# Performance work log

Hardware: AMD Instinct MI355X
Metric: run time of the kernel (lower is better)

The kernel has to match this reference:

```python
import jax, jax.numpy as jnp
import numpy as np

COMMITMENT_COST = 0.25


def _mlp(x, Ws, bs):
    # Linear layers with ReLU between hidden layers, linear output (rlpyt-style MlpModel).
    n = len(Ws)
    for i in range(n):
        x = x @ Ws[i] + bs[i]
        if i < n - 1:
            x = jax.nn.relu(x)
    return x


def setup_inputs() -> dict:
    key = jax.random.key(0)
    ks = jax.random.split(key, 16)
    B, D_in, H1, H2, D_code, K = 16384, 1024, 2048, 1024, 256, 1024

    def lin(kw, kb, fan_in, fan_out):
        lim = 1.0 / np.sqrt(fan_in)
        W = jax.random.uniform(kw, (fan_in, fan_out), jnp.float32, -lim, lim)
        b = jax.random.uniform(kb, (fan_out,), jnp.float32, -lim, lim)
        return W, b

    enc_W1, enc_b1 = lin(ks[0], ks[1], D_in, H1)
    enc_W2, enc_b2 = lin(ks[2], ks[3], H1, H2)
    enc_W3, enc_b3 = lin(ks[4], ks[5], H2, D_code)
    dec_W1, dec_b1 = lin(ks[6], ks[7], D_code, H2)
    dec_W2, dec_b2 = lin(ks[8], ks[9], H2, H1)
    dec_W3, dec_b3 = lin(ks[10], ks[11], H1, D_in)
    codebook = jax.random.uniform(ks[12], (K, D_code), jnp.float32, -1.0 / K, 1.0 / K)
    x = jax.random.normal(ks[13], (B, D_in), jnp.float32)
    return {
        "x": x,
        "enc_W1": enc_W1, "enc_b1": enc_b1,
        "enc_W2": enc_W2, "enc_b2": enc_b2,
        "enc_W3": enc_W3, "enc_b3": enc_b3,
        "codebook": codebook,
        "dec_W1": dec_W1, "dec_b1": dec_b1,
        "dec_W2": dec_W2, "dec_b2": dec_b2,
        "dec_W3": dec_W3, "dec_b3": dec_b3,
    }


def reference(x, enc_W1, enc_b1, enc_W2, enc_b2, enc_W3, enc_b3, codebook,
              dec_W1, dec_b1, dec_W2, dec_b2, dec_W3, dec_b3):
    # Encoder MLP -> z: [B, D_code]
    z = _mlp(x, [enc_W1, enc_W2, enc_W3], [enc_b1, enc_b2, enc_b3])
    # Squared L2 distances z vs codebook: [B, K]
    distances = (jnp.sum(z * z, axis=1, keepdims=True)
                 + jnp.sum(codebook * codebook, axis=1)
                 - 2.0 * jnp.einsum('bd,kd->bk', z, codebook))
    indices = jnp.argmin(distances, axis=1)  # [B]
    # one-hot scatter + matmul in the original == direct gather
    quantized = codebook[indices]            # [B, D_code]
    # training-mode losses
    e_latent_loss = jnp.mean((jax.lax.stop_gradient(quantized) - z) ** 2)
    q_latent_loss = jnp.mean((quantized - jax.lax.stop_gradient(z)) ** 2)
    loss = q_latent_loss + COMMITMENT_COST * e_latent_loss
    # straight-through estimator
    quantized_st = z + jax.lax.stop_gradient(quantized - z)
    reconstructed = _mlp(quantized_st, [dec_W1, dec_W2, dec_W3], [dec_b1, dec_b2, dec_b3])
    return reconstructed, quantized_st, loss, indices[:, None]
```

## Files before the change

### kernel.cpp

```cpp
#include <hip/hip_runtime.h>
#include <hip/hip_bf16.h>
#include <stdint.h>


#define BDIM  16384
#define DIN   1024
#define DH1   2048
#define DH2   1024
#define DCODE 256
#define KCODE 1024

typedef __hip_bfloat16 bf16;
typedef __attribute__((ext_vector_type(8))) short short8;
typedef __attribute__((ext_vector_type(4))) float f32x4;

__device__ __forceinline__ void gload16(const void* g, void* l)
{
    __builtin_amdgcn_global_load_lds(
        (const __attribute__((address_space(1))) unsigned int*)g,
        (__attribute__((address_space(3))) unsigned int*)l, 16, 0, 0);
}

__device__ __forceinline__ void split3(float f, ushort* h, ushort* m, ushort* l)
{
    bf16 bh = __float2bfloat16(f);
    float r1 = f - __bfloat162float(bh);
    bf16 bm = __float2bfloat16(r1);
    float r2 = r1 - __bfloat162float(bm);
    bf16 bl = __float2bfloat16(r2);
    *h = *(ushort*)&bh; *m = *(ushort*)&bm; *l = *(ushort*)&bl;
}

template<int RELU, int OUTK>
__global__ __launch_bounds__(512, 2)
void gemms(const ushort* __restrict__ Apl, const ushort* __restrict__ Bpl,
           const float* __restrict__ bias, void* __restrict__ C,
           void* __restrict__ C2,
           int M, int N, int K, size_t PA, size_t PB, size_t PC)
{
    __shared__ __align__(16) short As[2][3][128][32];
    __shared__ __align__(16) short Bs[2][3][128][32];
    const int tid  = threadIdx.x;
    const int lane = tid & 63;
    const int wave = tid >> 6;
    const int wm = (wave >> 1) << 5;
    const int wn = (wave & 1) << 6;
    const int fr = lane & 15, fq = lane >> 4;
    const int row0 = blockIdx.y << 7, col0 = blockIdx.x << 7;

    const int srow = (wave << 4) + (lane >> 2);
    const int sslot = lane & 3;
    const int skg = (sslot ^ ((srow >> 1) & 3)) << 3;

    const ushort* AgT = Apl + (size_t)(row0 + srow) * K + skg;
    const ushort* BgT = Bpl + (size_t)(col0 + srow) * K + skg;

    f32x4  acc[2][4];
    double dacc[2][4][4];
    #pragma unroll
    for (int i = 0; i < 2; ++i)
        #pragma unroll
        for (int j = 0; j < 4; ++j) {
            acc[i][j] = (f32x4)0.0f;
            #pragma unroll
            for (int r = 0; r < 4; ++r) dacc[i][j][r] = 0.0;
        }

    auto stage = [&](int b, int kb) {
        #pragma unroll
        for (int p = 0; p < 3; ++p) {
            gload16(AgT + (size_t)p * PA + kb, &As[b][p][wave << 4][0]);
            gload16(BgT + (size_t)p * PB + kb, &Bs[b][p][wave << 4][0]);
        }
    };

    stage(0, 0);
    const int nsteps = K >> 5;
    for (int s = 0; s < nsteps; ++s) {
        const int b = s & 1;
        if (s + 1 < nsteps) {
            stage(b ^ 1, (s + 1) << 5);
            asm volatile("s_waitcnt vmcnt(6)" ::: "memory");
        } else {
            asm volatile("s_waitcnt vmcnt(0)" ::: "memory");
        }
        __builtin_amdgcn_s_barrier();
        __builtin_amdgcn_sched_barrier(0);

        short8 bh[4], bm[4], bl[4];
        #pragma unroll
        for (int j = 0; j < 4; ++j) {
            const int bn = wn + (j << 4) + fr;
            const int bsl = (fq ^ ((bn >> 1) & 3)) << 3;
            bh[j] = *(const short8*)&Bs[b][0][bn][bsl];
            bm[j] = *(const short8*)&Bs[b][1][bn][bsl];
            bl[j] = *(const short8*)&Bs[b][2][bn][bsl];
        }
        #pragma unroll
        for (int i = 0; i < 2; ++i) {
            const int an = wm + (i << 4) + fr;
            const int asl = (fq ^ ((an >> 1) & 3)) << 3;
            short8 ah = *(const short8*)&As[b][0][an][asl];
            short8 am = *(const short8*)&As[b][1][an][asl];
            short8 al = *(const short8*)&As[b][2][an][asl];
            #pragma unroll
            for (int j = 0; j < 4; ++j) {
                acc[i][j] = __builtin_amdgcn_mfma_f32_16x16x32_bf16(ah, bh[j], acc[i][j], 0, 0, 0);
                acc[i][j] = __builtin_amdgcn_mfma_f32_16x16x32_bf16(ah, bm[j], acc[i][j], 0, 0, 0);
                acc[i][j] = __builtin_amdgcn_mfma_f32_16x16x32_bf16(am, bh[j], acc[i][j], 0, 0, 0);
                acc[i][j] = __builtin_amdgcn_mfma_f32_16x16x32_bf16(ah, bl[j], acc[i][j], 0, 0, 0);
                acc[i][j] = __builtin_amdgcn_mfma_f32_16x16x32_bf16(al, bh[j], acc[i][j], 0, 0, 0);
                acc[i][j] = __builtin_amdgcn_mfma_f32_16x16x32_bf16(am, bm[j], acc[i][j], 0, 0, 0);
            }
        }

        if (s & 1) {
            #pragma unroll
            for (int i = 0; i < 2; ++i)
                #pragma unroll
                for (int j = 0; j < 4; ++j) {
                    #pragma unroll
                    for (int r = 0; r < 4; ++r) dacc[i][j][r] += (double)acc[i][j][r];
                    acc[i][j] = (f32x4)0.0f;
                }
        }
        __builtin_amdgcn_sched_barrier(0);
        __builtin_amdgcn_s_barrier();
    }
    #pragma unroll
    for (int i = 0; i < 2; ++i)
        #pragma unroll
        for (int j = 0; j < 4; ++j)
            #pragma unroll
            for (int r = 0; r < 4; ++r) dacc[i][j][r] += (double)acc[i][j][r];

    #pragma unroll
    for (int j = 0; j < 4; ++j) {
        const int n = col0 + wn + (j << 4) + fr;
        const double bv = (double)bias[n];
        #pragma unroll
        for (int i = 0; i < 2; ++i) {
            const int mb = row0 + wm + (i << 4) + (fq << 2);
            #pragma unroll
            for (int r = 0; r < 4; ++r) {
                double v = dacc[i][j][r] + bv;
                if (RELU) v = v > 0.0 ? v : 0.0;
                const size_t o = (size_t)(mb + r) * N + n;
                if (OUTK == 2 || OUTK == 3) ((double*)C)[o] = v;
                if (OUTK == 0 || OUTK == 3) {
                    ushort h, m, l;
                    split3((float)v, &h, &m, &l);
                    ushort* Cp = (ushort*)((OUTK == 0) ? C : C2);
                    Cp[o] = h; Cp[PC + o] = m; Cp[2 * PC + o] = l;
                }
            }
        }
    }
}

__global__ __launch_bounds__(512, 2)
void distm(const ushort* __restrict__ Zpl, const ushort* __restrict__ Cpl,
           const double* __restrict__ c2, double* __restrict__ psc,
           int* __restrict__ pix)
{
    __shared__ __align__(16) short As[3][128][40];
    __shared__ __align__(16) short Bs[3][128][40];
    const int tid  = threadIdx.x;
    const int lane = tid & 63;
    const int wave = tid >> 6;
    const int wm = (wave >> 1) << 5;
    const int wn = (wave & 1) << 6;
    const int fr = lane & 15, fq = lane >> 4;
    const int row0 = blockIdx.y << 7, col0 = blockIdx.x << 7;
    const int sr = tid >> 2, sc = (tid & 3) << 3;
    const size_t PZ = (size_t)BDIM * DCODE;
    const size_t PC = (size_t)KCODE * DCODE;

    const ushort* Ag = Zpl + (size_t)(row0 + sr) * DCODE + sc;
    const ushort* Bg = Cpl + (size_t)(col0 + sr) * DCODE + sc;

    f32x4  acc[2][4];
    double dacc[2][4][4];
    #pragma unroll
    for (int i = 0; i < 2; ++i)
        #pragma unroll
        for (int j = 0; j < 4; ++j) {
            acc[i][j] = (f32x4)0.0f;
            #pragma unroll
            for (int r = 0; r < 4; ++r) dacc[i][j][r] = 0.0;
        }

    short8 sa[3], sb[3];
    #pragma unroll
    for (int p = 0; p < 3; ++p) {
        sa[p] = *(const short8*)(Ag + (size_t)p * PZ);
        sb[p] = *(const short8*)(Bg + (size_t)p * PC);
    }

    const int nsteps = DCODE >> 5;
    for (int s = 0; s < nsteps; ++s) {
        __syncthreads();
        #pragma unroll
        for (int p = 0; p < 3; ++p) {
            *(short8*)&As[p][sr][sc] = sa[p];
            *(short8*)&Bs[p][sr][sc] = sb[p];
        }
        __syncthreads();
        if (s + 1 < nsteps) {
            const int kb = (s + 1) << 5;
            #pragma unroll
            for (int p = 0; p < 3; ++p) {
                sa[p] = *(const short8*)(Ag + (size_t)p * PZ + kb);
                sb[p] = *(const short8*)(Bg + (size_t)p * PC + kb);
            }
        }

        short8 bh[4], bm[4], bl[4];
        #pragma unroll
        for (int j = 0; j < 4; ++j) {
            const int bn = wn + (j << 4) + fr;
            bh[j] = *(const short8*)&Bs[0][bn][fq << 3];
            bm[j] = *(const short8*)&Bs[1][bn][fq << 3];
            bl[j] = *(const short8*)&Bs[2][bn][fq << 3];
        }
        #pragma unroll
        for (int i = 0; i < 2; ++i) {
            const int an = wm + (i << 4) + fr;
            short8 ah = *(const short8*)&As[0][an][fq << 3];
            short8 am = *(const short8*)&As[1][an][fq << 3];
            short8 al = *(const short8*)&As[2][an][fq << 3];
            #pragma unroll
            for (int j = 0; j < 4; ++j) {
                acc[i][j] = __builtin_amdgcn_mfma_f32_16x16x32_bf16(ah, bh[j], acc[i][j], 0, 0, 0);
                acc[i][j] = __builtin_amdgcn_mfma_f32_16x16x32_bf16(ah, bm[j], acc[i][j], 0, 0, 0);
                acc[i][j] = __builtin_amdgcn_mfma_f32_16x16x32_bf16(am, bh[j], acc[i][j], 0, 0, 0);
                acc[i][j] = __builtin_amdgcn_mfma_f32_16x16x32_bf16(ah, bl[j], acc[i][j], 0, 0, 0);
                acc[i][j] = __builtin_amdgcn_mfma_f32_16x16x32_bf16(al, bh[j], acc[i][j], 0, 0, 0);
                acc[i][j] = __builtin_amdgcn_mfma_f32_16x16x32_bf16(am, bm[j], acc[i][j], 0, 0, 0);
            }
        }

        if (s & 1) {
            #pragma unroll
            for (int i = 0; i < 2; ++i)
                #pragma unroll
                for (int j = 0; j < 4; ++j) {
                    #pragma unroll
                    for (int r = 0; r < 4; ++r) dacc[i][j][r] += (double)acc[i][j][r];
                    acc[i][j] = (f32x4)0.0f;
                }
        }
    }
    #pragma unroll
    for (int i = 0; i < 2; ++i)
        #pragma unroll
        for (int j = 0; j < 4; ++j)
            #pragma unroll
            for (int r = 0; r < 4; ++r) dacc[i][j][r] += (double)acc[i][j][r];

    __syncthreads();
    double* scb = (double*)&As[0][0][0];
    int*    sib = (int*)(scb + 256);

    #pragma unroll
    for (int i = 0; i < 2; ++i) {
        #pragma unroll
        for (int r = 0; r < 4; ++r) {
            double bs = 1e300; int bi = 0;
            #pragma unroll
            for (int j = 0; j < 4; ++j) {
                const int n = col0 + wn + (j << 4) + fr;
                const double s = c2[n] - 2.0 * dacc[i][j][r];
                if (s < bs) { bs = s; bi = n; }
            }
            #pragma unroll
            for (int msk = 1; msk < 16; msk <<= 1) {
                double os = __shfl_xor(bs, msk, 64);
                int    oi = __shfl_xor(bi, msk, 64);
                if (os < bs || (os == bs && oi < bi)) { bs = os; bi = oi; }
            }
            if (fr == 0) {
                const int lr = wm + (i << 4) + (fq << 2) + r;
                scb[lr * 2 + (wave & 1)] = bs;
                sib[lr * 2 + (wave & 1)] = bi;
            }
        }
    }
    __syncthreads();
    if (tid < 128) {
        double s0 = scb[tid * 2], s1 = scb[tid * 2 + 1];
        int    i0 = sib[tid * 2], i1 = sib[tid * 2 + 1];
        const bool t1 = (s1 < s0) || (s1 == s0 && i1 < i0);
        const size_t o = (size_t)(row0 + tid) * (KCODE / 128) + blockIdx.x;
        psc[o] = t1 ? s1 : s0;
        pix[o] = t1 ? i1 : i0;
    }
}

__global__ __launch_bounds__(256)
void reduce8(const double* __restrict__ psc, const int* __restrict__ pix,
             int* __restrict__ idx_out)
{
    const int row = blockIdx.x * 256 + threadIdx.x;
    const double* ps = psc + (size_t)row * (KCODE / 128);
    const int*    pi = pix + (size_t)row * (KCODE / 128);
    double m = ps[0]; int mi = pi[0];
    #pragma unroll
    for (int t = 1; t < KCODE / 128; ++t) {
        double s = ps[t]; int c = pi[t];
        if (s < m || (s == m && c < mi)) { m = s; mi = c; }
    }
    idx_out[row] = mi;
}

template<int RELU, int OUTBF>
__global__ __launch_bounds__(256)
void gemmb2(const ushort* __restrict__ A, const ushort* __restrict__ Bt,
            const float* __restrict__ bias, void* __restrict__ C,
            int M, int N, int K)
{
    __shared__ __align__(16) short As[2][128][32];
    __shared__ __align__(16) short Bs[2][128][32];
    const int tid  = threadIdx.x;
    const int lane = tid & 63;
    const int wave = tid >> 6;
    const int wm = (wave >> 1) << 6, wn = (wave & 1) << 6;
    const int fr = lane & 15;
    const int fq = lane >> 4;
    const int row0 = blockIdx.y << 7, col0 = blockIdx.x << 7;

    const int sr0 = (wave << 5) + (lane >> 2);
    const int sslot = lane & 3;
    const int kg0 = (sslot ^ ((sr0 >> 1) & 3)) << 3;
    const int sr1 = sr0 + 16;
    const int kg1 = (sslot ^ ((sr1 >> 1) & 3)) << 3;

    const ushort* Ag0 = A  + (size_t)(row0 + sr0) * K + kg0;
    const ushort* Ag1 = A  + (size_t)(row0 + sr1) * K + kg1;
    const ushort* Bg0 = Bt + (size_t)(col0 + sr0) * K + kg0;
    const ushort* Bg1 = Bt + (size_t)(col0 + sr1) * K + kg1;

    f32x4 acc[4][4];
    #pragma unroll
    for (int i = 0; i < 4; ++i)
        #pragma unroll
        for (int j = 0; j < 4; ++j) acc[i][j] = (f32x4)0.0f;

    auto stage = [&](int b, int kb) {
        gload16(Ag0 + kb, &As[b][wave << 5][0]);
        gload16(Ag1 + kb, &As[b][(wave << 5) + 16][0]);
        gload16(Bg0 + kb, &Bs[b][wave << 5][0]);
        gload16(Bg1 + kb, &Bs[b][(wave << 5) + 16][0]);
    };

    stage(0, 0);
    const int nsteps = K >> 5;
    for (int s = 0; s < nsteps; ++s) {
        const int b = s & 1;
        if (s + 1 < nsteps) {
            stage(b ^ 1, (s + 1) << 5);
            asm volatile("s_waitcnt vmcnt(4)" ::: "memory");
        } else {
            asm volatile("s_waitcnt vmcnt(0)" ::: "memory");
        }
        __builtin_amdgcn_s_barrier();
        __builtin_amdgcn_sched_barrier(0);

        short8 af[4], bf[4];
        #pragma unroll
        for (int i = 0; i < 4; ++i) {
            const int an = wm + (i << 4) + fr;
            af[i] = *(const short8*)&As[b][an][(fq ^ ((an >> 1) & 3)) << 3];
        }
        #pragma unroll
        for (int j = 0; j < 4; ++j) {
            const int bn = wn + (j << 4) + fr;
            bf[j] = *(const short8*)&Bs[b][bn][(fq ^ ((bn >> 1) & 3)) << 3];
        }
        #pragma unroll
        for (int i = 0; i < 4; ++i)
            #pragma unroll
            for (int j = 0; j < 4; ++j)
                acc[i][j] = __builtin_amdgcn_mfma_f32_16x16x32_bf16(
                                af[i], bf[j], acc[i][j], 0, 0, 0);

        __builtin_amdgcn_sched_barrier(0);
        __builtin_amdgcn_s_barrier();
    }

    #pragma unroll
    for (int j = 0; j < 4; ++j) {
        const int n = col0 + wn + (j << 4) + fr;
        const float bv = bias[n];
        #pragma unroll
        for (int i = 0; i < 4; ++i) {
            const int mb = row0 + wm + (i << 4) + (fq << 2);
            #pragma unroll
            for (int r = 0; r < 4; ++r) {
                float v = acc[i][j][r] + bv;
                if (RELU) v = fmaxf(v, 0.0f);
                size_t o = (size_t)(mb + r) * N + n;
                if (OUTBF) ((bf16*)C)[o]  = __float2bfloat16(v);
                else       ((float*)C)[o] = v;
            }
        }
    }
}

__global__ __launch_bounds__(256)
void wtrans(const float* __restrict__ W, ushort* __restrict__ Wt, int K, int N)
{
    __shared__ float tile[64][65];
    const int tid = threadIdx.x;
    const int kb = blockIdx.y << 6, nb = blockIdx.x << 6;
    const int r = tid >> 4, c4 = (tid & 15) << 2;
    #pragma unroll
    for (int s = 0; s < 4; ++s) {
        float4 v = *(const float4*)(W + (size_t)(kb + r + (s << 4)) * N + nb + c4);
        tile[r + (s << 4)][c4 + 0] = v.x; tile[r + (s << 4)][c4 + 1] = v.y;
        tile[r + (s << 4)][c4 + 2] = v.z; tile[r + (s << 4)][c4 + 3] = v.w;
    }
    __syncthreads();
    #pragma unroll
    for (int s = 0; s < 4; ++s) {
        const int n = r + (s << 4);
        ushort u[4];
        #pragma unroll
        for (int l = 0; l < 4; ++l) {
            bf16 h = __float2bfloat16(tile[c4 + l][n]);
            u[l] = *(ushort*)&h;
        }
        *(ushort4*)(Wt + (size_t)(nb + n) * K + kb + c4) = make_ushort4(u[0], u[1], u[2], u[3]);
    }
}

__global__ __launch_bounds__(256)
void wsplit(const float* __restrict__ W, ushort* __restrict__ Wt, int K, int N)
{
    __shared__ float tile[64][65];
    const int tid = threadIdx.x;
    const int kb = blockIdx.y << 6, nb = blockIdx.x << 6;
    const int r = tid >> 4, c4 = (tid & 15) << 2;
    const size_t NK = (size_t)N * K;
    #pragma unroll
    for (int s = 0; s < 4; ++s) {
        float4 v = *(const float4*)(W + (size_t)(kb + r + (s << 4)) * N + nb + c4);
        tile[r + (s << 4)][c4 + 0] = v.x; tile[r + (s << 4)][c4 + 1] = v.y;
        tile[r + (s << 4)][c4 + 2] = v.z; tile[r + (s << 4)][c4 + 3] = v.w;
    }
    __syncthreads();
    #pragma unroll
    for (int s = 0; s < 4; ++s) {
        const int n = r + (s << 4);
        ushort h[4], m[4], l[4];
        #pragma unroll
        for (int e = 0; e < 4; ++e) split3(tile[c4 + e][n], &h[e], &m[e], &l[e]);
        const size_t o = (size_t)(nb + n) * K + kb + c4;
        *(ushort4*)(Wt + o)          = make_ushort4(h[0], h[1], h[2], h[3]);
        *(ushort4*)(Wt + NK + o)     = make_ushort4(m[0], m[1], m[2], m[3]);
        *(ushort4*)(Wt + 2 * NK + o) = make_ushort4(l[0], l[1], l[2], l[3]);
    }
}

__global__ __launch_bounds__(256)
void xsplit(const float* __restrict__ X, ushort* __restrict__ Xp, size_t P)
{
    const size_t i = ((size_t)blockIdx.x * 256 + threadIdx.x) << 2;
    float4 v = *(const float4*)(X + i);
    ushort h[4], m[4], l[4];
    split3(v.x, &h[0], &m[0], &l[0]);
    split3(v.y, &h[1], &m[1], &l[1]);
    split3(v.z, &h[2], &m[2], &l[2]);
    split3(v.w, &h[3], &m[3], &l[3]);
    *(ushort4*)(Xp + i)         = make_ushort4(h[0], h[1], h[2], h[3]);
    *(ushort4*)(Xp + P + i)     = make_ushort4(m[0], m[1], m[2], m[3]);
    *(ushort4*)(Xp + 2 * P + i) = make_ushort4(l[0], l[1], l[2], l[3]);
}

__global__ __launch_bounds__(64)
void c2_k(const float* __restrict__ cb, double* __restrict__ c2)
{
    int code = blockIdx.x, l = threadIdx.x;
    float4 v = *(const float4*)(cb + (size_t)code * DCODE + (l << 2));
    double s = (double)v.x * v.x + (double)v.y * v.y
             + (double)v.z * v.z + (double)v.w * v.w;
    #pragma unroll
    for (int off = 32; off; off >>= 1) s += __shfl_down(s, off, 64);
    if (l == 0) c2[code] = s;
}

__global__ __launch_bounds__(256)
void gather_k(const int* __restrict__ idx_in, const float* __restrict__ cb,
              const double* __restrict__ z, ushort* __restrict__ qstb,
              float* __restrict__ out_qst, float* __restrict__ out_idx,
              double* __restrict__ psum)
{
    const int tid  = threadIdx.x;
    const int row  = (blockIdx.x << 2) + (tid >> 6);
    const int lane = tid & 63;
    const int d    = lane << 2;
    const int idx  = idx_in[row];

    float4 qv = *(const float4*)(cb + (size_t)idx * DCODE + d);
    const double* zp = z + (size_t)row * DCODE + d;
    double2 z0 = *(const double2*)(zp);
    double2 z1 = *(const double2*)(zp + 2);

    double q[4] = {(double)qv.x, (double)qv.y, (double)qv.z, (double)qv.w};
    double zz[4] = {z0.x, z0.y, z1.x, z1.y};
    double qs[4];
    double s = 0.0;
    #pragma unroll
    for (int e = 0; e < 4; ++e) {
        double diff = q[e] - zz[e];
        qs[e] = zz[e] + diff;
        s += diff * diff;
    }
    *(float4*)(out_qst + (size_t)row * DCODE + d) =
        make_float4((float)qs[0], (float)qs[1], (float)qs[2], (float)qs[3]);
    ushort u[4];
    #pragma unroll
    for (int e = 0; e < 4; ++e) {
        bf16 h = __float2bfloat16((float)qs[e]);
        u[e] = *(ushort*)&h;
    }
    *(ushort4*)(qstb + (size_t)row * DCODE + d) = make_ushort4(u[0], u[1], u[2], u[3]);

    #pragma unroll
    for (int off = 32; off; off >>= 1) s += __shfl_down(s, off, 64);
    __shared__ double sred[4];
    if (lane == 0) {
        sred[tid >> 6] = s;
        out_idx[row] = (float)idx;
    }
    __syncthreads();
    if (tid == 0) psum[blockIdx.x] = sred[0] + sred[1] + sred[2] + sred[3];
}

__global__ __launch_bounds__(256)
void loss_k(const double* __restrict__ psum, float* __restrict__ out_loss)
{
    const int tid = threadIdx.x;
    double s = 0.0;
    for (int i = tid; i < BDIM / 4; i += 256) s += psum[i];
    #pragma unroll
    for (int off = 32; off; off >>= 1) s += __shfl_down(s, off, 64);
    __shared__ double sred[4];
    if ((tid & 63) == 0) sred[tid >> 6] = s;
    __syncthreads();
    if (tid == 0)
        out_loss[0] = (float)(1.25 * (sred[0] + sred[1] + sred[2] + sred[3]) / 4194304.0);
}

extern "C" void kernel_launch(void* const* d_in, const int* in_sizes, int n_in,
                              void* d_out, int out_size, void* d_ws, size_t ws_size,
                              hipStream_t stream)
{
    const float* x   = (const float*)d_in[0];
    const float* eW1 = (const float*)d_in[1];
    const float* eb1 = (const float*)d_in[2];
    const float* eW2 = (const float*)d_in[3];
    const float* eb2 = (const float*)d_in[4];
    const float* eW3 = (const float*)d_in[5];
    const float* eb3 = (const float*)d_in[6];
    const float* cbk = (const float*)d_in[7];
    const float* dW1 = (const float*)d_in[8];
    const float* db1 = (const float*)d_in[9];
    const float* dW2 = (const float*)d_in[10];
    const float* db2 = (const float*)d_in[11];
    const float* dW3 = (const float*)d_in[12];
    const float* db3 = (const float*)d_in[13];

    const size_t EPS1 = (size_t)3 * 2048 * 1024 * 2;
    const size_t EPS2 = (size_t)3 * 1024 * 2048 * 2;
    const size_t EPS3 = (size_t)3 * 256 * 1024 * 2;
    const size_t EPS  = EPS1 + EPS2 + EPS3;
    const size_t FIX_W1 = (size_t)1024 * 256 * 2;
    const size_t FIX_W2 = (size_t)2048 * 1024 * 2;
    const size_t FIX_W3 = (size_t)1024 * 2048 * 2;
    const size_t ZB   = (size_t)BDIM * DCODE * 8;
    const size_t ZPLB = (size_t)3 * BDIM * DCODE * 2;
    const size_t QSTB = (size_t)BDIM * DCODE * 2;
    const size_t IDXB = (size_t)BDIM * 4;
    const size_t NPT  = KCODE / 128;
    const size_t PSCB = (size_t)BDIM * NPT * 8;
    const size_t PIXB = (size_t)BDIM * NPT * 4;
    const size_t CBPB = (size_t)3 * KCODE * DCODE * 2;
    const size_t PSUM = (size_t)(BDIM / 4) * 8;

    const size_t PERSIST = FIX_W1 + FIX_W2 + FIX_W3 + ZB + ZPLB + QSTB + IDXB
                         + PSCB + PIXB + CBPB + PSUM + 8192 + 256;

    int R = BDIM;
    while (R > 256 && PERSIST + EPS + (size_t)R * 24576 > ws_size) R >>= 1;
    const int nch = BDIM / R;

    char* ws = (char*)d_ws;
    size_t off = 0;
    ushort* eP1  = (ushort*)(ws + off); off += EPS1;
    ushort* eP2  = (ushort*)(ws + off); off += EPS2;
    ushort* eP3  = (ushort*)(ws + off); off += EPS3;
    ushort* xpl  = (ushort*)(ws + off); off += (size_t)R * 6144;
    ushort* h1pl = (ushort*)(ws + off); off += (size_t)R * 12288;
    ushort* h2pl = (ushort*)(ws + off); off += (size_t)R * 6144;
    ushort* dh1b = xpl;
    ushort* dh2b = h1pl;
    ushort* Wt1  = (ushort*)(ws + off); off += FIX_W1;
    ushort* Wt2  = (ushort*)(ws + off); off += FIX_W2;
    ushort* Wt3  = (ushort*)(ws + off); off += FIX_W3;
    double* zb   = (double*)(ws + off); off += ZB;
    ushort* zpl  = (ushort*)(ws + off); off += ZPLB;
    ushort* qstb = (ushort*)(ws + off); off += QSTB;
    int*    idxb = (int*)(ws + off);    off += IDXB;
    double* psc  = (double*)(ws + off); off += PSCB;
    int*    pix  = (int*)(ws + off);    off += PIXB;
    ushort* cbP  = (ushort*)(ws + off); off += CBPB;
    double* psum = (double*)(ws + off); off += PSUM;
    double* c2   = (double*)(ws + off); off += 8192;

    float* out      = (float*)d_out;
    float* out_rec  = out;
    float* out_qst  = out + (size_t)BDIM * DIN;
    float* out_loss = out_qst + (size_t)BDIM * DCODE;
    float* out_idx  = out_loss + 1;

    c2_k<<<KCODE, 64, 0, stream>>>(cbk, c2);
    wtrans<<<dim3(1024 / 64,  256 / 64), 256, 0, stream>>>(dW1, Wt1,  256, 1024);
    wtrans<<<dim3(2048 / 64, 1024 / 64), 256, 0, stream>>>(dW2, Wt2, 1024, 2048);
    wtrans<<<dim3(1024 / 64, 2048 / 64), 256, 0, stream>>>(dW3, Wt3, 2048, 1024);
    wsplit<<<dim3(2048 / 64, 1024 / 64), 256, 0, stream>>>(eW1, eP1, 1024, 2048);
    wsplit<<<dim3(1024 / 64, 2048 / 64), 256, 0, stream>>>(eW2, eP2, 2048, 1024);
    wsplit<<<dim3( 256 / 64, 1024 / 64), 256, 0, stream>>>(eW3, eP3, 1024,  256);
    xsplit<<<(KCODE * DCODE) / 1024, 256, 0, stream>>>(cbk, cbP, (size_t)KCODE * DCODE);

    for (int c = 0; c < nch; ++c) {
        const float* xc = x + (size_t)c * R * DIN;
        double* zb_c  = zb + (size_t)c * R * DCODE;
        ushort* zpl_c = zpl + (size_t)c * R * DCODE;
        xsplit<<<R, 256, 0, stream>>>(xc, xpl, (size_t)R * DIN);
        gemms<1, 0><<<dim3(DH1 / 128, R / 128), 512, 0, stream>>>(
            xpl, eP1, eb1, h1pl, nullptr, R, DH1, DIN,
            (size_t)R * DIN, (size_t)DH1 * DIN, (size_t)R * DH1);
        gemms<1, 0><<<dim3(DH2 / 128, R / 128), 512, 0, stream>>>(
            h1pl, eP2, eb2, h2pl, nullptr, R, DH2, DH1,
            (size_t)R * DH1, (size_t)DH2 * DH1, (size_t)R * DH2);
        gemms<0, 3><<<dim3(DCODE / 128, R / 128), 512, 0, stream>>>(
            h2pl, eP3, eb3, zb_c, zpl_c, R, DCODE, DH2,
            (size_t)R * DH2, (size_t)DCODE * DH2, (size_t)BDIM * DCODE);
    }

    distm<<<dim3(KCODE / 128, BDIM / 128), 512, 0, stream>>>(zpl, cbP, c2, psc, pix);
    reduce8<<<BDIM / 256, 256, 0, stream>>>(psc, pix, idxb);

    gather_k<<<BDIM / 4, 256, 0, stream>>>(idxb, cbk, zb, qstb, out_qst, out_idx, psum);

    for (int c = 0; c < nch; ++c) {
        const ushort* qst_c = qstb + (size_t)c * R * DCODE;
        float* rec_c = out_rec + (size_t)c * R * DIN;
        gemmb2<1, 1><<<dim3(DH2 / 128, R / 128), 256, 0, stream>>>(qst_c, Wt1, db1, dh1b, R, DH2, DCODE);
        gemmb2<1, 1><<<dim3(DH1 / 128, R / 128), 256, 0, stream>>>(dh1b, Wt2, db2, dh2b, R, DH1, DH2);
        gemmb2<0, 0><<<dim3(DIN / 128, R / 128), 256, 0, stream>>>(dh2b, Wt3, db3, rec_c, R, DIN, DH1);
    }

    loss_k<<<1, 256, 0, stream>>>(psum, out_loss);
}
```

Measured before the change: 1.588 ms.

## Triple-buffer GEMM LDS staging and swizzle block order across XCDs

The gemms and gemmb2 kernels move from double to triple-buffered LDS staging, keeping two k-tiles of global-to-LDS loads in flight with adjusted vmcnt waits. All GEMM and distance kernels switch to a 1D grid whose block index is remapped so that consecutive blocks spread across the 8 XCDs, aiming for better L2 locality of the shared operand tiles. The cost is more LDS per block: gemms grows to about 72KB, which may hurt the intended 2-blocks-per-CU occupancy. The new index mapping and wait counts must match the load counts exactly.

```diff
diff --git a/kernel.cpp b/kernel.cpp
--- a/kernel.cpp
+++ b/kernel.cpp
@@ -21,6 +21,15 @@
         (__attribute__((address_space(3))) unsigned int*)l, 16, 0, 0);
 }
 
+__device__ __forceinline__ void swz_xcd(int gxlog, int* bx, int* by)
+{
+    unsigned wg = blockIdx.x;
+    const unsigned nwg = gridDim.x;
+    if ((nwg & 7u) == 0u) wg = (wg & 7u) * (nwg >> 3) + (wg >> 3);
+    *bx = wg & ((1u << gxlog) - 1u);
+    *by = wg >> gxlog;
+}
+
 __device__ __forceinline__ void split3(float f, ushort* h, ushort* m, ushort* l)
 {
     bf16 bh = __float2bfloat16(f);
@@ -36,17 +45,19 @@
 void gemms(const ushort* __restrict__ Apl, const ushort* __restrict__ Bpl,
            const float* __restrict__ bias, void* __restrict__ C,
            void* __restrict__ C2,
-           int M, int N, int K, size_t PA, size_t PB, size_t PC)
-{
-    __shared__ __align__(16) short As[2][3][128][32];
-    __shared__ __align__(16) short Bs[2][3][128][32];
+           int M, int N, int K, size_t PA, size_t PB, size_t PC, int gxlog)
+{
+    __shared__ __align__(16) short As[3][3][128][32];
+    __shared__ __align__(16) short Bs[3][3][128][32];
     const int tid  = threadIdx.x;
     const int lane = tid & 63;
     const int wave = tid >> 6;
     const int wm = (wave >> 1) << 5;
     const int wn = (wave & 1) << 6;
     const int fr = lane & 15, fq = lane >> 4;
-    const int row0 = blockIdx.y << 7, col0 = blockIdx.x << 7;
+    int bx, by;
+    swz_xcd(gxlog, &bx, &by);
+    const int row0 = by << 7, col0 = bx << 7;
 
     const int srow = (wave << 4) + (lane >> 2);
     const int sslot = lane & 3;
@@ -75,11 +86,15 @@
     };
 
     stage(0, 0);
+    stage(1, 32);
     const int nsteps = K >> 5;
+    int b = 0, sb = 2;
     for (int s = 0; s < nsteps; ++s) {
-        const int b = s & 1;
-        if (s + 1 < nsteps) {
-            stage(b ^ 1, (s + 1) << 5);
+        if (s + 2 < nsteps) {
+            stage(sb, (s + 2) << 5);
+            sb = (sb == 2) ? 0 : sb + 1;
+            asm volatile("s_waitcnt vmcnt(12)" ::: "memory");
+        } else if (s + 1 < nsteps) {
             asm volatile("s_waitcnt vmcnt(6)" ::: "memory");
         } else {
             asm volatile("s_waitcnt vmcnt(0)" ::: "memory");
@@ -124,6 +139,7 @@
                     acc[i][j] = (f32x4)0.0f;
                 }
         }
+        b = (b == 2) ? 0 : b + 1;
         __builtin_amdgcn_sched_barrier(0);
         __builtin_amdgcn_s_barrier();
     }
@@ -171,7 +187,9 @@
     const int wm = (wave >> 1) << 5;
     const int wn = (wave & 1) << 6;
     const int fr = lane & 15, fq = lane >> 4;
-    const int row0 = blockIdx.y << 7, col0 = blockIdx.x << 7;
+    int bx, by;
+    swz_xcd(3, &bx, &by);
+    const int row0 = by << 7, col0 = bx << 7;
     const int sr = tid >> 2, sc = (tid & 3) << 3;
     const size_t PZ = (size_t)BDIM * DCODE;
     const size_t PC = (size_t)KCODE * DCODE;
@@ -291,7 +309,7 @@
         double s0 = scb[tid * 2], s1 = scb[tid * 2 + 1];
         int    i0 = sib[tid * 2], i1 = sib[tid * 2 + 1];
         const bool t1 = (s1 < s0) || (s1 == s0 && i1 < i0);
-        const size_t o = (size_t)(row0 + tid) * (KCODE / 128) + blockIdx.x;
+        const size_t o = (size_t)(row0 + tid) * (KCODE / 128) + bx;
         psc[o] = t1 ? s1 : s0;
         pix[o] = t1 ? i1 : i0;
     }
@@ -317,17 +335,19 @@
 __global__ __launch_bounds__(256)
 void gemmb2(const ushort* __restrict__ A, const ushort* __restrict__ Bt,
             const float* __restrict__ bias, void* __restrict__ C,
-            int M, int N, int K)
-{
-    __shared__ __align__(16) short As[2][128][32];
-    __shared__ __align__(16) short Bs[2][128][32];
+            int M, int N, int K, int gxlog)
+{
+    __shared__ __align__(16) short As[3][128][32];
+    __shared__ __align__(16) short Bs[3][128][32];
     const int tid  = threadIdx.x;
     const int lane = tid & 63;
     const int wave = tid >> 6;
     const int wm = (wave >> 1) << 6, wn = (wave & 1) << 6;
     const int fr = lane & 15;
     const int fq = lane >> 4;
-    const int row0 = blockIdx.y << 7, col0 = blockIdx.x << 7;
+    int bx, by;
+    swz_xcd(gxlog, &bx, &by);
+    const int row0 = by << 7, col0 = bx << 7;
 
     const int sr0 = (wave << 5) + (lane >> 2);
     const int sslot = lane & 3;
@@ -354,11 +374,15 @@
     };
 
     stage(0, 0);
+    stage(1, 32);
     const int nsteps = K >> 5;
+    int b = 0, sbuf = 2;
     for (int s = 0; s < nsteps; ++s) {
-        const int b = s & 1;
-        if (s + 1 < nsteps) {
-            stage(b ^ 1, (s + 1) << 5);
+        if (s + 2 < nsteps) {
+            stage(sbuf, (s + 2) << 5);
+            sbuf = (sbuf == 2) ? 0 : sbuf + 1;
+            asm volatile("s_waitcnt vmcnt(8)" ::: "memory");
+        } else if (s + 1 < nsteps) {
             asm volatile("s_waitcnt vmcnt(4)" ::: "memory");
         } else {
             asm volatile("s_waitcnt vmcnt(0)" ::: "memory");
@@ -384,6 +408,7 @@
                 acc[i][j] = __builtin_amdgcn_mfma_f32_16x16x32_bf16(
                                 af[i], bf[j], acc[i][j], 0, 0, 0);
 
+        b = (b == 2) ? 0 : b + 1;
         __builtin_amdgcn_sched_barrier(0);
         __builtin_amdgcn_s_barrier();
     }
@@ -633,23 +658,25 @@
     wsplit<<<dim3( 256 / 64, 1024 / 64), 256, 0, stream>>>(eW3, eP3, 1024,  256);
     xsplit<<<(KCODE * DCODE) / 1024, 256, 0, stream>>>(cbk, cbP, (size_t)KCODE * DCODE);
 
+    const int rb = R / 128;
+
     for (int c = 0; c < nch; ++c) {
         const float* xc = x + (size_t)c * R * DIN;
         double* zb_c  = zb + (size_t)c * R * DCODE;
         ushort* zpl_c = zpl + (size_t)c * R * DCODE;
         xsplit<<<R, 256, 0, stream>>>(xc, xpl, (size_t)R * DIN);
-        gemms<1, 0><<<dim3(DH1 / 128, R / 128), 512, 0, stream>>>(
+        gemms<1, 0><<<16 * rb, 512, 0, stream>>>(
             xpl, eP1, eb1, h1pl, nullptr, R, DH1, DIN,
-            (size_t)R * DIN, (size_t)DH1 * DIN, (size_t)R * DH1);
-        gemms<1, 0><<<dim3(DH2 / 128, R / 128), 512, 0, stream>>>(
+            (size_t)R * DIN, (size_t)DH1 * DIN, (size_t)R * DH1, 4);
+        gemms<1, 0><<<8 * rb, 512, 0, stream>>>(
             h1pl, eP2, eb2, h2pl, nullptr, R, DH2, DH1,
-            (size_t)R * DH1, (size_t)DH2 * DH1, (size_t)R * DH2);
-        gemms<0, 3><<<dim3(DCODE / 128, R / 128), 512, 0, stream>>>(
+            (size_t)R * DH1, (size_t)DH2 * DH1, (size_t)R * DH2, 3);
+        gemms<0, 3><<<2 * rb, 512, 0, stream>>>(
             h2pl, eP3, eb3, zb_c, zpl_c, R, DCODE, DH2,
-            (size_t)R * DH2, (size_t)DCODE * DH2, (size_t)BDIM * DCODE);
-    }
-
-    distm<<<dim3(KCODE / 128, BDIM / 128), 512, 0, stream>>>(zpl, cbP, c2, psc, pix);
+            (size_t)R * DH2, (size_t)DCODE * DH2, (size_t)BDIM * DCODE, 1);
+    }
+
+    distm<<<8 * (BDIM / 128), 512, 0, stream>>>(zpl, cbP, c2, psc, pix);
     reduce8<<<BDIM / 256, 256, 0, stream>>>(psc, pix, idxb);
 
     gather_k<<<BDIM / 4, 256, 0, stream>>>(idxb, cbk, zb, qstb, out_qst, out_idx, psum);
@@ -657,9 +684,9 @@
     for (int c = 0; c < nch; ++c) {
         const ushort* qst_c = qstb + (size_t)c * R * DCODE;
         float* rec_c = out_rec + (size_t)c * R * DIN;
-        gemmb2<1, 1><<<dim3(DH2 / 128, R / 128), 256, 0, stream>>>(qst_c, Wt1, db1, dh1b, R, DH2, DCODE);
-        gemmb2<1, 1><<<dim3(DH1 / 128, R / 128), 256, 0, stream>>>(dh1b, Wt2, db2, dh2b, R, DH1, DH2);
-        gemmb2<0, 0><<<dim3(DIN / 128, R / 128), 256, 0, stream>>>(dh2b, Wt3, db3, rec_c, R, DIN, DH1);
+        gemmb2<1, 1><<<8 * rb, 256, 0, stream>>>(qst_c, Wt1, db1, dh1b, R, DH2, DCODE, 3);
+        gemmb2<1, 1><<<16 * rb, 256, 0, stream>>>(dh1b, Wt2, db2, dh2b, R, DH1, DH2, 4);
+        gemmb2<0, 0><<<8 * rb, 256, 0, stream>>>(dh2b, Wt3, db3, rec_c, R, DIN, DH1, 3);
     }
 
     loss_k<<<1, 256, 0, stream>>>(psum, out_loss);
```

Result: faster. 1.550 ms (-2.4%).
